# Kernel optimization log

Hardware: AMD Instinct MI355X
Metric: run time of the kernel (lower is better)

The kernel has to match this reference:

```python
import jax, jax.numpy as jnp
import numpy as np

N, E, C, NTT, NMOL = 200000, 1600000, 128, 20000, 2000
EPS = 1e-5


def setup_inputs() -> dict:
    key = jax.random.key(0)
    ks = jax.random.split(key, 32)
    s = 0.05
    d = {}
    d["node_attr"] = jax.random.normal(ks[0], (N, C), jnp.float32)
    d["adj_index"] = jax.random.randint(ks[1], (2, E), 0, N)
    d["adj_value"] = jax.random.uniform(ks[2], (E,), jnp.float32)
    d["tt_node_batch"] = jnp.sort(jax.random.randint(ks[3], (N,), 0, NTT))
    d["tt_graph_batch"] = jnp.sort(jax.random.randint(ks[4], (NTT,), 0, NMOL))
    # GCN layers (2): linear weight/bias
    d["W_gcn"] = jax.random.normal(ks[5], (2, C, C)) * s
    d["b_gcn"] = jnp.zeros((2, C))
    # 8 BatchNorm1d(C): [gcn0, gcn1, tt0, tt1, tt2, mol0, mol1, mol2] (eval mode)
    d["bn_gamma"] = jnp.ones((8, C))
    d["bn_beta"] = jnp.zeros((8, C))
    d["bn_mean"] = jnp.zeros((8, C))
    d["bn_var"] = jnp.ones((8, C))
    # 2 GATConv (tt, mol): bipartite lin_src/lin_dst, att_src/att_dst, bias (heads=1)
    d["gat_Wsrc"] = jax.random.normal(ks[6], (2, C, C)) * s
    d["gat_Wdst"] = jax.random.normal(ks[7], (2, C, C)) * s
    d["gat_asrc"] = jax.random.normal(ks[8], (2, C)) * s
    d["gat_adst"] = jax.random.normal(ks[9], (2, C)) * s
    d["gat_bias"] = jnp.zeros((2, C))
    # 2 GRUCell(C, C)
    d["gru_Wih"] = jax.random.normal(ks[10], (2, 3 * C, C)) * s
    d["gru_Whh"] = jax.random.normal(ks[11], (2, 3 * C, C)) * s
    d["gru_bih"] = jnp.zeros((2, 3 * C))
    d["gru_bhh"] = jnp.zeros((2, 3 * C))
    # predictor: 128 -> 64 (relu) -> 1
    d["pW1"] = jax.random.normal(ks[12], (64, C)) * s
    d["pb1"] = jnp.full((64,), 0.01)
    d["pW2"] = jax.random.normal(ks[13], (1, 64)) * s
    d["pb2"] = jnp.full((1,), 0.01)
    return d


def _bn(x, i, g, b, m, v):
    return (x - m[i]) * (g[i] / jnp.sqrt(v[i] + EPS)) + b[i]


def _spmm(idx, val, x, n):  # out[i] = sum_j A[i,j] x[j]
    return jax.ops.segment_sum(val[:, None] * x[idx[1]], idx[0], num_segments=n)


def _gat(x_src, x_dst, src, dst, nseg, Ws, Wd, a_s, a_d, bias):
    hs = x_src @ Ws.T
    hd = x_dst @ Wd.T
    alpha = jax.nn.leaky_relu(hs @ a_s, 0.01 * 0 + 0.01) if False else None
    a = (hs @ a_s)[src] + (hd @ a_d)[dst]
    a = jnp.where(a > 0, a, 0.01 * a)  # leaky_relu, negative_slope=0.01
    mx = jax.ops.segment_max(a, dst, num_segments=nseg)
    e = jnp.exp(a - mx[dst])
    den = jax.ops.segment_sum(e, dst, num_segments=nseg)
    w = e / den[dst]
    return jax.ops.segment_sum(w[:, None] * hs[src], dst, num_segments=nseg) + bias


def _gru(x, h, Wih, Whh, bih, bhh):
    gi = x @ Wih.T + bih
    gh = h @ Whh.T + bhh
    ir, iz, inn = jnp.split(gi, 3, axis=-1)
    hr, hz, hn = jnp.split(gh, 3, axis=-1)
    r = jax.nn.sigmoid(ir + hr)
    z = jax.nn.sigmoid(iz + hz)
    n = jnp.tanh(inn + r * hn)
    return (1.0 - z) * n + z * h


def _pool_stage(x, seg, nseg, bn_base, gi, bn_gamma, bn_beta, bn_mean, bn_var,
                gat_Wsrc, gat_Wdst, gat_asrc, gat_adst, gat_bias,
                gru_Wih, gru_Whh, gru_bih, gru_bhh):
    x = _bn(x, bn_base, bn_gamma, bn_beta, bn_mean, bn_var)
    mean = jax.ops.segment_sum(x, seg, num_segments=nseg)  # global_add_pool
    mean = _bn(jax.nn.relu(mean), bn_base + 1, bn_gamma, bn_beta, bn_mean, bn_var)
    src = jnp.arange(x.shape[0])
    g = _gat(x, mean, src, seg, nseg, gat_Wsrc[gi], gat_Wdst[gi], gat_asrc[gi], gat_adst[gi], gat_bias[gi])
    g = jax.nn.elu(g)  # dropout p=0.001 is identity in eval
    g = _gru(g, mean, gru_Wih[gi], gru_Whh[gi], gru_bih[gi], gru_bhh[gi])
    return _bn(jax.nn.relu(g), bn_base + 2, bn_gamma, bn_beta, bn_mean, bn_var)


def reference(node_attr, adj_value, W_gcn, b_gcn, bn_gamma, bn_beta, bn_mean, bn_var,
              gat_Wsrc, gat_Wdst, gat_asrc, gat_adst, gat_bias,
              gru_Wih, gru_Whh, gru_bih, gru_bhh, pW1, pb1, pW2, pb2,
              adj_index, tt_node_batch, tt_graph_batch):
    # graph embedder: two GCN layers  x <- relu(BN(A @ (x W^T) + b))
    x = node_attr
    for i in range(2):
        x = _spmm(adj_index, adj_value, x @ W_gcn[i].T, N) + b_gcn[i]
        x = jax.nn.relu(_bn(x, i, bn_gamma, bn_beta, bn_mean, bn_var))
    # tt pooling: nodes -> tt subgraphs
    tt = _pool_stage(x, tt_node_batch, NTT, 2, 0, bn_gamma, bn_beta, bn_mean, bn_var,
                     gat_Wsrc, gat_Wdst, gat_asrc, gat_adst, gat_bias,
                     gru_Wih, gru_Whh, gru_bih, gru_bhh)
    # mol pooling: tt subgraphs -> molecules
    mol = _pool_stage(tt, tt_graph_batch, NMOL, 5, 1, bn_gamma, bn_beta, bn_mean, bn_var,
                      gat_Wsrc, gat_Wdst, gat_asrc, gat_adst, gat_bias,
                      gru_Wih, gru_Whh, gru_bih, gru_bhh)
    # predictor
    h = jax.nn.relu(mol @ pW1.T + pb1)
    return h @ pW2.T + pb2  # [NMOL, 1]
```

## Files before the change

kernel.cpp:

```cpp
#include <hip/hip_runtime.h>
#include <math.h>

#define CCH 128
#define G3  384
#define BN_EPS 1e-5f
#define BSH 9
#define BROWS 512

typedef __bf16 bf16;
typedef __bf16 bf16x2 __attribute__((ext_vector_type(2)));
typedef __bf16 bf16x4 __attribute__((ext_vector_type(4)));
typedef __bf16 bf16x8 __attribute__((ext_vector_type(8)));
typedef float f32x4 __attribute__((ext_vector_type(4)));


__global__ void bnprep_kernel(const float* __restrict__ g, const float* __restrict__ b,
                              const float* __restrict__ m, const float* __restrict__ v,
                              float* __restrict__ sc, float* __restrict__ sh)
{
    int idx = blockIdx.x * 128 + threadIdx.x;
    float s = g[idx] / sqrtf(v[idx] + BN_EPS);
    sc[idx] = s;
    sh[idx] = b[idx] - m[idx] * s;
}

__global__ void f2b_kernel(const float* __restrict__ in, bf16* __restrict__ out, int n4)
{
    int i = blockIdx.x * 256 + threadIdx.x;
    if (i >= n4) return;
    float4 v = ((const float4*)in)[i];
    bf16x4 o = { (bf16)v.x, (bf16)v.y, (bf16)v.z, (bf16)v.w };
    ((bf16x4*)out)[i] = o;
}

__global__ __launch_bounds__(128) void matvec_prep_kernel(
    const float* __restrict__ Wsrc, const float* __restrict__ Wdst,
    const float* __restrict__ asrc, const float* __restrict__ adst,
    const float* __restrict__ bnsc, const float* __restrict__ bnsh,
    float* __restrict__ vsp, float* __restrict__ vd, float* __restrict__ c0)
{
    __shared__ float red[2];
    int s = blockIdx.x >> 1, which = blockIdx.x & 1;
    int k = threadIdx.x;
    const float* W = (which ? Wdst : Wsrc) + s * CCH * CCH;
    const float* a = (which ? adst : asrc) + s * CCH;
    float acc = 0.f;
    for (int j = 0; j < CCH; ++j) acc += W[j * CCH + k] * a[j];
    if (which) {
        vd[s * CCH + k] = acc;
    } else {
        int l = 2 + 3 * s;
        vsp[s * CCH + k] = acc * bnsc[l * CCH + k];
        float p = bnsh[l * CCH + k] * acc;
        for (int o = 32; o; o >>= 1) p += __shfl_down(p, o);
        if ((k & 63) == 0) red[k >> 6] = p;
        __syncthreads();
        if (k == 0) c0[s] = red[0] + red[1];
    }
}

__global__ void bounds_kernel(const int* __restrict__ batch, int n, int nseg, int* __restrict__ starts)
{
    int s = blockIdx.x * 256 + threadIdx.x;
    if (s > nseg) return;
    int lo = 0, hi = n;
    while (lo < hi) {
        int mid = (lo + hi) >> 1;
        if (batch[mid] < s) lo = mid + 1; else hi = mid;
    }
    starts[s] = lo;
}


__global__ __launch_bounds__(256) void bucket_hist_kernel(const int* __restrict__ rows,
                                                          int* __restrict__ bhist, int E)
{
    __shared__ int h[512];
    int t = threadIdx.x;
    h[t] = 0; h[t + 256] = 0;
    __syncthreads();
    int base = blockIdx.x * 4096;
#pragma unroll
    for (int i = 0; i < 16; ++i) {
        int e = base + i * 256 + t;
        if (e < E) atomicAdd(&h[rows[e] >> BSH], 1);
    }
    __syncthreads();
    if (h[t]) atomicAdd(&bhist[t], h[t]);
    if (h[t + 256]) atomicAdd(&bhist[t + 256], h[t + 256]);
}

__global__ __launch_bounds__(256) void bucket_scan_kernel(const int* __restrict__ bhist,
                                                          int* __restrict__ boff, int* __restrict__ bcur,
                                                          int* __restrict__ row_ptr, int NB, int N, int E)
{
    __shared__ int h[512], sx[512], wt[4];
    int t = threadIdx.x;
    h[t] = bhist[t]; h[t + 256] = bhist[t + 256];
    __syncthreads();
    int v0 = h[2 * t], v1 = h[2 * t + 1];
    int s = v0 + v1, incl = s;
    for (int o = 1; o < 64; o <<= 1) { int u = __shfl_up(incl, o); if ((t & 63) >= o) incl += u; }
    if ((t & 63) == 63) wt[t >> 6] = incl;
    __syncthreads();
    int woff = 0, w = t >> 6;
    for (int i = 0; i < w; ++i) woff += wt[i];
    int excl = woff + incl - s;
    sx[2 * t] = excl; sx[2 * t + 1] = excl + v0;
    __syncthreads();
    if (t < NB)       { boff[t] = sx[t];       bcur[t] = sx[t]; }
    if (t + 256 < NB) { boff[t + 256] = sx[t + 256]; bcur[t + 256] = sx[t + 256]; }
    if (t == 0) { boff[NB] = E; row_ptr[N] = E; }
}

__global__ __launch_bounds__(256) void bucket_bin_kernel(
    const int* __restrict__ rows, const int* __restrict__ cols, const float* __restrict__ val,
    int* __restrict__ bcur, int* __restrict__ brow, int2* __restrict__ bcv, int E)
{
    __shared__ int hist[512], sx[512], cnt[512], gbase[512], wt[4];
    __shared__ int mrow[4096];
    __shared__ int2 mcv[4096];
    int t = threadIdx.x;
    hist[t] = 0; hist[t + 256] = 0; cnt[t] = 0; cnt[t + 256] = 0;
    __syncthreads();
    int base = blockIdx.x * 4096;
    int r[16];
#pragma unroll
    for (int i = 0; i < 16; ++i) {
        int e = base + i * 256 + t;
        r[i] = (e < E) ? rows[e] : -1;
        if (r[i] >= 0) atomicAdd(&hist[r[i] >> BSH], 1);
    }
    __syncthreads();
    int v0 = hist[2 * t], v1 = hist[2 * t + 1];
    int s = v0 + v1, incl = s;
    for (int o = 1; o < 64; o <<= 1) { int u = __shfl_up(incl, o); if ((t & 63) >= o) incl += u; }
    if ((t & 63) == 63) wt[t >> 6] = incl;
    __syncthreads();
    int woff = 0, w = t >> 6;
    for (int i = 0; i < w; ++i) woff += wt[i];
    int excl = woff + incl - s;
    sx[2 * t] = excl; sx[2 * t + 1] = excl + v0;
    __syncthreads();
    for (int b = t; b < 512; b += 256)
        if (hist[b]) gbase[b] = atomicAdd(&bcur[b], hist[b]);
    __syncthreads();
#pragma unroll
    for (int i = 0; i < 16; ++i) {
        if (r[i] < 0) continue;
        int e = base + i * 256 + t;
        int b = r[i] >> BSH;
        int p = atomicAdd(&cnt[b], 1);
        int loc = sx[b] + p;
        mrow[loc] = r[i];
        int2 cv; cv.x = cols[e]; cv.y = __float_as_int(val[e]);
        mcv[loc] = cv;
    }
    __syncthreads();
    int Mv = sx[511] + hist[511];
    for (int loc = t; loc < Mv; loc += 256) {
        int b = mrow[loc] >> BSH;
        int g = gbase[b] + (loc - sx[b]);
        brow[g] = mrow[loc];
        bcv[g]  = mcv[loc];
    }
}

__global__ __launch_bounds__(256) void bucket_place_kernel(
    const int* __restrict__ brow, const int2* __restrict__ bcv,
    const int* __restrict__ boff, int* __restrict__ row_ptr,
    int2* __restrict__ cpack, int N)
{
    __shared__ int rcnt[512], sx[512], wt[4];
    int b = blockIdx.x;
    int t = threadIdx.x;
    rcnt[t] = 0; rcnt[t + 256] = 0;
    __syncthreads();
    int rbase = b << BSH;
    int rn = min(BROWS, N - rbase);
    int lo = boff[b], hi = boff[b + 1];
    for (int p = lo + t; p < hi; p += 256)
        atomicAdd(&rcnt[brow[p] - rbase], 1);
    __syncthreads();
    int v0 = rcnt[2 * t], v1 = rcnt[2 * t + 1];
    int s = v0 + v1, incl = s;
    for (int o = 1; o < 64; o <<= 1) { int u = __shfl_up(incl, o); if ((t & 63) >= o) incl += u; }
    if ((t & 63) == 63) wt[t >> 6] = incl;
    __syncthreads();
    int woff = 0, w = t >> 6;
    for (int i = 0; i < w; ++i) woff += wt[i];
    int excl = woff + incl - s;
    sx[2 * t] = excl; sx[2 * t + 1] = excl + v0;
    __syncthreads();
    if (t < rn)       row_ptr[rbase + t] = lo + sx[t];
    if (t + 256 < rn) row_ptr[rbase + t + 256] = lo + sx[t + 256];
    __syncthreads();
    sx[t] += lo; sx[t + 256] += lo;
    __syncthreads();
    for (int p = lo + t; p < hi; p += 256) {
        int r = brow[p];
        int slot = atomicAdd(&sx[r - rbase], 1);
        cpack[slot] = bcv[p];
    }
}


template<int IN_BF16, int OUT_BF16, int ACT>
__global__ __launch_bounds__(256, 2) void gemm_mfma(
    const void* __restrict__ Xv, const bf16* __restrict__ W,
    const float* __restrict__ bias, void* __restrict__ Yv, int M, int Nout)
{
    __shared__ bf16 Xs[128 * 136];
    __shared__ bf16 Ws[128 * 136];
    const int tid = threadIdx.x;
    const int rb = blockIdx.x * 128;
    const int cb = blockIdx.y * 128;

#pragma unroll
    for (int i = 0; i < 8; ++i) {
        int c = tid + i * 256;
        int r = c >> 4, k8 = (c & 15) << 3;
        *(bf16x8*)&Ws[r * 136 + k8] = *(const bf16x8*)&W[(size_t)(cb + r) * CCH + k8];
    }
    if (IN_BF16) {
#pragma unroll
        for (int i = 0; i < 8; ++i) {
            int c = tid + i * 256;
            int r = c >> 4, k8 = (c & 15) << 3;
            int grow = rb + r;
            bf16x8 o = {};
            if (grow < M) o = *(const bf16x8*)&((const bf16*)Xv)[(size_t)grow * CCH + k8];
            *(bf16x8*)&Xs[r * 136 + k8] = o;
        }
    } else {
#pragma unroll
        for (int i = 0; i < 16; ++i) {
            int c = tid + i * 256;
            int r = c >> 5, k4 = (c & 31) << 2;
            int grow = rb + r;
            bf16x4 o = {};
            if (grow < M) {
                float4 xv = *(const float4*)&((const float*)Xv)[(size_t)grow * CCH + k4];
                o[0] = (bf16)xv.x; o[1] = (bf16)xv.y; o[2] = (bf16)xv.z; o[3] = (bf16)xv.w;
            }
            *(bf16x4*)&Xs[r * 136 + k4] = o;
        }
    }
    __syncthreads();

    const int w = tid >> 6, lane = tid & 63;
    const int col16 = lane & 15, quad = lane >> 4;
    const int wm = (w & 1) * 64, wn = (w >> 1) * 64;

    f32x4 acc[4][4] = {};
#pragma unroll
    for (int kk = 0; kk < 4; ++kk) {
        bf16x8 af[4], bfr[4];
#pragma unroll
        for (int mi = 0; mi < 4; ++mi)
            af[mi] = *(const bf16x8*)&Xs[(wm + mi * 16 + col16) * 136 + kk * 32 + quad * 8];
#pragma unroll
        for (int ni = 0; ni < 4; ++ni)
            bfr[ni] = *(const bf16x8*)&Ws[(wn + ni * 16 + col16) * 136 + kk * 32 + quad * 8];
#pragma unroll
        for (int mi = 0; mi < 4; ++mi)
#pragma unroll
            for (int ni = 0; ni < 4; ++ni)
                acc[mi][ni] = __builtin_amdgcn_mfma_f32_16x16x32_bf16(af[mi], bfr[ni], acc[mi][ni], 0, 0, 0);
    }

#pragma unroll
    for (int mi = 0; mi < 4; ++mi) {
#pragma unroll
        for (int r = 0; r < 4; ++r) {
            int row = rb + wm + mi * 16 + quad * 4 + r;
            if (row >= M) continue;
#pragma unroll
            for (int ni = 0; ni < 4; ++ni) {
                int col = cb + wn + ni * 16 + col16;
                float v = acc[mi][ni][r];
                if (bias) v += bias[col];
                if (ACT == 1) v = v > 0.f ? v : expm1f(v);
                if (OUT_BF16) ((bf16*)Yv)[(size_t)row * Nout + col] = (bf16)v;
                else          ((float*)Yv)[(size_t)row * Nout + col] = v;
            }
        }
    }
}

template<int SCORES>
__global__ __launch_bounds__(256) void spmm_csr_kernel(
    const int* __restrict__ row_ptr, const int2* __restrict__ cpack,
    const bf16* __restrict__ Xin, bf16* __restrict__ Y,
    const float* __restrict__ bvec, const float* __restrict__ sc, const float* __restrict__ sh,
    const float* __restrict__ vsp, const float* __restrict__ c0p, float* __restrict__ scores,
    int Nrow)
{
    int gid = blockIdx.x * 256 + threadIdx.x;
    int row = gid >> 4;
    if (row >= Nrow) return;
    int l8 = (gid & 15) << 3;
    int st = row_ptr[row], en = row_ptr[row + 1];
    float acc[8] = {};
    int j = st;
    for (; j + 2 <= en; j += 2) {
        int2 p0 = cpack[j];
        int2 p1 = cpack[j + 1];
        bf16x8 x0 = *(const bf16x8*)&Xin[(size_t)p0.x * CCH + l8];
        bf16x8 x1 = *(const bf16x8*)&Xin[(size_t)p1.x * CCH + l8];
        float v0 = __int_as_float(p0.y), v1 = __int_as_float(p1.y);
#pragma unroll
        for (int q = 0; q < 8; ++q) acc[q] += v0 * (float)x0[q] + v1 * (float)x1[q];
    }
    if (j < en) {
        int2 p0 = cpack[j];
        bf16x8 x0 = *(const bf16x8*)&Xin[(size_t)p0.x * CCH + l8];
        float v0 = __int_as_float(p0.y);
#pragma unroll
        for (int q = 0; q < 8; ++q) acc[q] += v0 * (float)x0[q];
    }
    float o[8];
    bf16x8 ov;
#pragma unroll
    for (int q = 0; q < 8; ++q) {
        o[q] = fmaxf((acc[q] + bvec[l8 + q]) * sc[l8 + q] + sh[l8 + q], 0.f);
        ov[q] = (bf16)o[q];
    }
    *(bf16x8*)&Y[(size_t)row * CCH + l8] = ov;
    if (SCORES) {
        float p = 0.f;
#pragma unroll
        for (int q = 0; q < 8; ++q) p += o[q] * vsp[l8 + q];
        for (int d = 8; d; d >>= 1) p += __shfl_down(p, d, 16);
        if ((gid & 15) == 0) scores[row] = p + c0p[0];
    }
}

__global__ __launch_bounds__(128) void segstage_kernel(
    const bf16* __restrict__ X, const float* __restrict__ sarr, const int* __restrict__ starts,
    const float* __restrict__ sc2, const float* __restrict__ sh2,
    const float* __restrict__ sc3, const float* __restrict__ sh3,
    const float* __restrict__ vd, float* __restrict__ mean, float* __restrict__ upool)
{
    __shared__ float red[2];
    __shared__ float adsh;
    int t = blockIdx.x;
    int c = threadIdx.x;
    int st = starts[t], en = starts[t + 1];
    float sum = 0.f;
    for (int i = st; i < en; ++i) sum += (float)X[(size_t)i * CCH + c];
    float cnt = (float)(en - st);
    float poolb = fmaxf(sum * sc2[c] + cnt * sh2[c], 0.f);
    float mv = poolb * sc3[c] + sh3[c];
    mean[(size_t)t * CCH + c] = mv;
    float p = mv * vd[c];
    for (int o = 32; o; o >>= 1) p += __shfl_down(p, o);
    if ((c & 63) == 0) red[c >> 6] = p;
    __syncthreads();
    if (c == 0) adsh = red[0] + red[1];
    __syncthreads();
    if (en == st) { upool[(size_t)t * CCH + c] = 0.f; return; }
    float adt = adsh;
    float lm = -3.0e38f;
    for (int i = st + c; i < en; i += 128) {
        float a = sarr[i] + adt;
        a = a > 0.f ? a : 0.01f * a;
        lm = fmaxf(lm, a);
    }
    for (int o = 32; o; o >>= 1) lm = fmaxf(lm, __shfl_down(lm, o));
    if ((c & 63) == 0) red[c >> 6] = lm;
    __syncthreads();
    float m = fmaxf(red[0], red[1]);
    float u = 0.f, den = 0.f;
    for (int i = st; i < en; ++i) {
        float a = sarr[i] + adt;
        a = a > 0.f ? a : 0.01f * a;
        float e = __expf(a - m);
        den += e;
        u += e * (float)X[(size_t)i * CCH + c];
    }
    upool[(size_t)t * CCH + c] = (u / den) * sc2[c] + sh2[c];
}

template<int OUT_BF16, int SCORES>
__global__ __launch_bounds__(256) void gru_kernel(
    const float* __restrict__ giM, const float* __restrict__ ghM, const float* __restrict__ mean,
    const float* __restrict__ sc4, const float* __restrict__ sh4,
    void* __restrict__ out,
    const float* __restrict__ vsp2, const float* __restrict__ c02, float* __restrict__ scores,
    int total)
{
    __shared__ float sred[4];
    int idx = blockIdx.x * 256 + threadIdx.x;
    bool ok = idx < total;
    int t = idx >> 7, c = idx & 127;
    float o = 0.f;
    if (ok) {
        size_t b = (size_t)t * G3;
        float ir = giM[b + c],  iz = giM[b + 128 + c], inn = giM[b + 256 + c];
        float hr = ghM[b + c],  hz = ghM[b + 128 + c], hn  = ghM[b + 256 + c];
        float r = 1.f / (1.f + __expf(-(ir + hr)));
        float z = 1.f / (1.f + __expf(-(iz + hz)));
        float nn = tanhf(inn + r * hn);
        float h = (1.f - z) * nn + z * mean[idx];
        h = fmaxf(h, 0.f);
        o = h * sc4[c] + sh4[c];
        if (OUT_BF16) ((bf16*)out)[idx] = (bf16)o;
        else          ((float*)out)[idx] = o;
    }
    if (SCORES) {
        float p = ok ? o * vsp2[c] : 0.f;
        for (int d = 32; d; d >>= 1) p += __shfl_down(p, d);
        int w = threadIdx.x >> 6;
        if ((threadIdx.x & 63) == 0) sred[w] = p;
        __syncthreads();
        if (threadIdx.x == 0 && ok)   scores[t] = sred[0] + sred[1] + c02[0];
        if (threadIdx.x == 128 && ok) scores[t] = sred[2] + sred[3] + c02[0];
    }
}

__global__ __launch_bounds__(64) void pred_kernel(
    const float* __restrict__ mol, const float* __restrict__ pW1, const float* __restrict__ pb1,
    const float* __restrict__ pW2, const float* __restrict__ pb2, float* __restrict__ out)
{
    __shared__ float row[CCH];
    int m = blockIdx.x;
    int j = threadIdx.x;
    row[j] = mol[(size_t)m * CCH + j];
    row[j + 64] = mol[(size_t)m * CCH + 64 + j];
    __syncthreads();
    float h = pb1[j];
#pragma unroll
    for (int k = 0; k < CCH; ++k) h += row[k] * pW1[j * CCH + k];
    h = fmaxf(h, 0.f);
    float p = h * pW2[j];
    for (int o = 32; o; o >>= 1) p += __shfl_down(p, o);
    if (j == 0) out[m] = p + pb2[0];
}


extern "C" void kernel_launch(void* const* d_in, const int* in_sizes, int n_in,
                              void* d_out, int out_size, void* d_ws, size_t ws_size,
                              hipStream_t stream)
{
    (void)n_in; (void)ws_size;
    const float* node_attr      = (const float*)d_in[0];
    const int*   adj_index      = (const int*)  d_in[1];
    const float* adj_value      = (const float*)d_in[2];
    const int*   tt_node_batch  = (const int*)  d_in[3];
    const int*   tt_graph_batch = (const int*)  d_in[4];
    const float* W_gcn    = (const float*)d_in[5];
    const float* b_gcn    = (const float*)d_in[6];
    const float* bn_gamma = (const float*)d_in[7];
    const float* bn_beta  = (const float*)d_in[8];
    const float* bn_mean  = (const float*)d_in[9];
    const float* bn_var   = (const float*)d_in[10];
    const float* gat_Wsrc = (const float*)d_in[11];
    const float* gat_Wdst = (const float*)d_in[12];
    const float* gat_asrc = (const float*)d_in[13];
    const float* gat_adst = (const float*)d_in[14];
    const float* gat_bias = (const float*)d_in[15];
    const float* gru_Wih  = (const float*)d_in[16];
    const float* gru_Whh  = (const float*)d_in[17];
    const float* gru_bih  = (const float*)d_in[18];
    const float* gru_bhh  = (const float*)d_in[19];
    const float* pW1 = (const float*)d_in[20];
    const float* pb1 = (const float*)d_in[21];
    const float* pW2 = (const float*)d_in[22];
    const float* pb2 = (const float*)d_in[23];

    const int E    = in_sizes[2];
    const int N    = in_sizes[3];
    const int NTT  = in_sizes[4];
    const int NMOL = out_size;
    const int NB   = (N + BROWS - 1) >> BSH;

    const int* adj_rows = adj_index;
    const int* adj_cols = adj_index + E;

    char* wsb = (char*)d_ws;
    size_t off = 0;
    auto carve = [&](size_t bytes) -> char* {
        char* p = wsb + off;
        off = (off + bytes + 255) & ~(size_t)255;
        return p;
    };
    bf16* bufB = (bf16*)carve((size_t)N * CCH * 2);
    bf16* bufA = (bf16*)carve((size_t)N * CCH * 2);
    bf16* tt   = (bf16*)carve((size_t)NTT * CCH * 2);
    float* mol  = (float*)carve((size_t)NMOL * CCH * 4);
    float* mean  = (float*)carve((size_t)NTT * CCH * 4);
    float* upool = (float*)carve((size_t)NTT * CCH * 4);
    float* gbuf  = (float*)carve((size_t)NTT * CCH * 4);
    float* giM   = (float*)carve((size_t)NTT * G3 * 4);
    float* ghM   = (float*)carve((size_t)NTT * G3 * 4);
    float* scores = (float*)carve((size_t)N * 4);
    int* starts_tt  = (int*)carve((size_t)(NTT + 1) * 4);
    int* starts_mol = (int*)carve((size_t)(NMOL + 1) * 4);
    float* bnsc = (float*)carve(8 * CCH * 4);
    float* bnsh = (float*)carve(8 * CCH * 4);
    float* vsp  = (float*)carve(2 * CCH * 4);
    float* vd   = (float*)carve(2 * CCH * 4);
    float* c0   = (float*)carve(2 * 4);
    bf16* Wgcnb = (bf16*)carve((size_t)2 * CCH * CCH * 2);
    bf16* Wsrcb = (bf16*)carve((size_t)2 * CCH * CCH * 2);
    bf16* Wihb  = (bf16*)carve((size_t)2 * G3 * CCH * 2);
    bf16* Whhb  = (bf16*)carve((size_t)2 * G3 * CCH * 2);
    int*   bhist   = (int*)carve(512 * 4);
    int*   boff    = (int*)carve((size_t)(NB + 1) * 4);
    int*   bcur    = (int*)carve((size_t)NB * 4);
    int*   row_ptr = (int*)carve((size_t)(N + 1) * 4);
    int*   brow    = (int*)carve((size_t)E * 4);
    int2*  bcv     = (int2*)carve((size_t)E * 8);
    int2*  cpack   = (int2*)carve((size_t)E * 8);

    bnprep_kernel<<<8, 128, 0, stream>>>(bn_gamma, bn_beta, bn_mean, bn_var, bnsc, bnsh);
    matvec_prep_kernel<<<4, 128, 0, stream>>>(gat_Wsrc, gat_Wdst, gat_asrc, gat_adst,
                                              bnsc, bnsh, vsp, vd, c0);
    {
        int n4;
        n4 = 2 * CCH * CCH / 4; f2b_kernel<<<(n4 + 255) / 256, 256, 0, stream>>>(W_gcn, Wgcnb, n4);
        n4 = 2 * CCH * CCH / 4; f2b_kernel<<<(n4 + 255) / 256, 256, 0, stream>>>(gat_Wsrc, Wsrcb, n4);
        n4 = 2 * G3 * CCH / 4;  f2b_kernel<<<(n4 + 255) / 256, 256, 0, stream>>>(gru_Wih, Wihb, n4);
        n4 = 2 * G3 * CCH / 4;  f2b_kernel<<<(n4 + 255) / 256, 256, 0, stream>>>(gru_Whh, Whhb, n4);
    }
    bounds_kernel<<<(NTT + 1 + 255) / 256, 256, 0, stream>>>(tt_node_batch, N, NTT, starts_tt);
    bounds_kernel<<<(NMOL + 1 + 255) / 256, 256, 0, stream>>>(tt_graph_batch, NTT, NMOL, starts_mol);

    const int nchunk = (E + 4095) / 4096;
    hipMemsetAsync(bhist, 0, 512 * 4, stream);
    bucket_hist_kernel<<<nchunk, 256, 0, stream>>>(adj_rows, bhist, E);
    bucket_scan_kernel<<<1, 256, 0, stream>>>(bhist, boff, bcur, row_ptr, NB, N, E);
    bucket_bin_kernel<<<nchunk, 256, 0, stream>>>(adj_rows, adj_cols, adj_value,
                                                  bcur, brow, bcv, E);
    bucket_place_kernel<<<NB, 256, 0, stream>>>(brow, bcv, boff, row_ptr, cpack, N);

    dim3 gg((N + 127) / 128, 1);
    const int spmm_blocks = ((size_t)N * 16 + 255) / 256;
    gemm_mfma<0, 1, 0><<<gg, 256, 0, stream>>>(node_attr, Wgcnb, nullptr, bufB, N, CCH);
    spmm_csr_kernel<0><<<spmm_blocks, 256, 0, stream>>>(
        row_ptr, cpack, bufB, bufA, b_gcn, bnsc, bnsh, nullptr, nullptr, nullptr, N);
    gemm_mfma<1, 1, 0><<<gg, 256, 0, stream>>>(bufA, Wgcnb + CCH * CCH, nullptr, bufB, N, CCH);
    spmm_csr_kernel<1><<<spmm_blocks, 256, 0, stream>>>(
        row_ptr, cpack, bufB, bufA, b_gcn + CCH, bnsc + CCH, bnsh + CCH,
        vsp, c0, scores, N);

    {
        int bnb = 2, gi = 0, nseg = NTT;
        segstage_kernel<<<nseg, 128, 0, stream>>>(bufA, scores, starts_tt,
            bnsc + bnb * CCH, bnsh + bnb * CCH, bnsc + (bnb + 1) * CCH, bnsh + (bnb + 1) * CCH,
            vd + gi * CCH, mean, upool);
        dim3 g1((nseg + 127) / 128, 1);
        gemm_mfma<0, 0, 1><<<g1, 256, 0, stream>>>(upool, Wsrcb + gi * CCH * CCH,
                                                   gat_bias + gi * CCH, gbuf, nseg, CCH);
        dim3 g2((nseg + 127) / 128, 3);
        gemm_mfma<0, 0, 0><<<g2, 256, 0, stream>>>(gbuf, Wihb + gi * G3 * CCH,
                                                   gru_bih + gi * G3, giM, nseg, G3);
        gemm_mfma<0, 0, 0><<<g2, 256, 0, stream>>>(mean, Whhb + gi * G3 * CCH,
                                                   gru_bhh + gi * G3, ghM, nseg, G3);
        gru_kernel<1, 1><<<(nseg * CCH + 255) / 256, 256, 0, stream>>>(giM, ghM, mean,
            bnsc + (bnb + 2) * CCH, bnsh + (bnb + 2) * CCH, tt,
            vsp + CCH, c0 + 1, scores, nseg * CCH);
    }

    {
        int bnb = 5, gi = 1, nseg = NMOL;
        segstage_kernel<<<nseg, 128, 0, stream>>>(tt, scores, starts_mol,
            bnsc + bnb * CCH, bnsh + bnb * CCH, bnsc + (bnb + 1) * CCH, bnsh + (bnb + 1) * CCH,
            vd + gi * CCH, mean, upool);
        dim3 g1((nseg + 127) / 128, 1);
        gemm_mfma<0, 0, 1><<<g1, 256, 0, stream>>>(upool, Wsrcb + gi * CCH * CCH,
                                                   gat_bias + gi * CCH, gbuf, nseg, CCH);
        dim3 g2((nseg + 127) / 128, 3);
        gemm_mfma<0, 0, 0><<<g2, 256, 0, stream>>>(gbuf, Wihb + gi * G3 * CCH,
                                                   gru_bih + gi * G3, giM, nseg, G3);
        gemm_mfma<0, 0, 0><<<g2, 256, 0, stream>>>(mean, Whhb + gi * G3 * CCH,
                                                   gru_bhh + gi * G3, ghM, nseg, G3);
        gru_kernel<0, 0><<<(nseg * CCH + 255) / 256, 256, 0, stream>>>(giM, ghM, mean,
            bnsc + (bnb + 2) * CCH, bnsh + (bnb + 2) * CCH, mol,
            nullptr, nullptr, nullptr, nseg * CCH);
    }

    pred_kernel<<<NMOL, 64, 0, stream>>>(mol, pW1, pb1, pW2, pb2, (float*)d_out);
}
```

Baseline: 688.6 us.

## Fuse prep kernels, pack row into column bits, merge GRU GEMMs and predictor

Merges the BN prep, matvec prep, bounds search, histogram memset and weight bf16 conversions into one multi-role launch. Drops the separate row array in CSR construction by packing the in-bucket row index into the high bits of the column word. Fuses the two GRU GEMMs into a single dual launch and fuses the final GRU with the predictor MLP. It also unrolls the SpMM inner loop to four edges. The aim is fewer launches and less memory traffic in the preprocessing, at the cost of relying on column indices fitting in 19 bits.

```diff
diff --git a/kernel.cpp b/kernel.cpp
--- a/kernel.cpp
+++ b/kernel.cpp
@@ -6,6 +6,7 @@
 #define BN_EPS 1e-5f
 #define BSH 9
 #define BROWS 512
+#define COLBITS 19
 
 typedef __bf16 bf16;
 typedef __bf16 bf16x2 __attribute__((ext_vector_type(2)));
@@ -13,62 +14,81 @@
 typedef __bf16 bf16x8 __attribute__((ext_vector_type(8)));
 typedef float f32x4 __attribute__((ext_vector_type(4)));
 
-
-__global__ void bnprep_kernel(const float* __restrict__ g, const float* __restrict__ b,
-                              const float* __restrict__ m, const float* __restrict__ v,
-                              float* __restrict__ sc, float* __restrict__ sh)
-{
-    int idx = blockIdx.x * 128 + threadIdx.x;
-    float s = g[idx] / sqrtf(v[idx] + BN_EPS);
-    sc[idx] = s;
-    sh[idx] = b[idx] - m[idx] * s;
-}
-
-__global__ void f2b_kernel(const float* __restrict__ in, bf16* __restrict__ out, int n4)
-{
-    int i = blockIdx.x * 256 + threadIdx.x;
-    if (i >= n4) return;
-    float4 v = ((const float4*)in)[i];
-    bf16x4 o = { (bf16)v.x, (bf16)v.y, (bf16)v.z, (bf16)v.w };
-    ((bf16x4*)out)[i] = o;
-}
-
-__global__ __launch_bounds__(128) void matvec_prep_kernel(
+__global__ __launch_bounds__(256) void prep_kernel(
+    const float* __restrict__ g, const float* __restrict__ b,
+    const float* __restrict__ m, const float* __restrict__ v,
+    float* __restrict__ bnsc, float* __restrict__ bnsh,
     const float* __restrict__ Wsrc, const float* __restrict__ Wdst,
     const float* __restrict__ asrc, const float* __restrict__ adst,
-    const float* __restrict__ bnsc, const float* __restrict__ bnsh,
-    float* __restrict__ vsp, float* __restrict__ vd, float* __restrict__ c0)
+    float* __restrict__ vsp, float* __restrict__ vd, float* __restrict__ c0,
+    const int* __restrict__ tt_node_batch, int N, int NTT, int* __restrict__ starts_tt,
+    const int* __restrict__ tt_graph_batch, int NMOL, int* __restrict__ starts_mol,
+    int* __restrict__ bhist,
+    const float* __restrict__ Wgcn, bf16* __restrict__ Wgcnb,
+    bf16* __restrict__ Wsrcb,
+    const float* __restrict__ Wih, bf16* __restrict__ Wihb,
+    const float* __restrict__ Whh, bf16* __restrict__ Whhb,
+    int B1, int B2, int B3, int B4, int B5, int B6, int B7, int B8)
 {
     __shared__ float red[2];
-    int s = blockIdx.x >> 1, which = blockIdx.x & 1;
-    int k = threadIdx.x;
-    const float* W = (which ? Wdst : Wsrc) + s * CCH * CCH;
-    const float* a = (which ? adst : asrc) + s * CCH;
-    float acc = 0.f;
-    for (int j = 0; j < CCH; ++j) acc += W[j * CCH + k] * a[j];
-    if (which) {
-        vd[s * CCH + k] = acc;
+    const int bid = blockIdx.x;
+    const int tid = threadIdx.x;
+    if (bid < B1) {
+        int idx = bid * 256 + tid;
+        if (idx < 8 * CCH) {
+            float s = g[idx] / sqrtf(v[idx] + BN_EPS);
+            bnsc[idx] = s;
+            bnsh[idx] = b[idx] - m[idx] * s;
+        }
+    } else if (bid < B2) {
+        int s = bid - B1;
+        int which = tid >> 7, k = tid & 127;
+        const float* W = (which ? Wdst : Wsrc) + s * CCH * CCH;
+        const float* a = (which ? adst : asrc) + s * CCH;
+        float acc = 0.f;
+        for (int j = 0; j < CCH; ++j) acc += W[j * CCH + k] * a[j];
+        if (which) {
+            vd[s * CCH + k] = acc;
+        } else {
+            int l = 2 + 3 * s;
+            float scl = g[l * CCH + k] / sqrtf(v[l * CCH + k] + BN_EPS);
+            float shf = b[l * CCH + k] - m[l * CCH + k] * scl;
+            vsp[s * CCH + k] = acc * scl;
+            float p = shf * acc;
+            for (int o = 32; o; o >>= 1) p += __shfl_down(p, o);
+            if ((k & 63) == 0) red[k >> 6] = p;
+        }
+        __syncthreads();
+        if (tid == 0) c0[s] = red[0] + red[1];
+    } else if (bid < B3) {
+        int s = (bid - B2) * 256 + tid;
+        if (s <= NTT) {
+            int lo = 0, hi = N;
+            while (lo < hi) { int mid = (lo + hi) >> 1; if (tt_node_batch[mid] < s) lo = mid + 1; else hi = mid; }
+            starts_tt[s] = lo;
+        }
+    } else if (bid < B4) {
+        int s = (bid - B3) * 256 + tid;
+        if (s <= NMOL) {
+            int lo = 0, hi = NTT;
+            while (lo < hi) { int mid = (lo + hi) >> 1; if (tt_graph_batch[mid] < s) lo = mid + 1; else hi = mid; }
+            starts_mol[s] = lo;
+        }
+    } else if (bid < B5) {
+        bhist[tid] = 0; bhist[tid + 256] = 0;
     } else {
-        int l = 2 + 3 * s;
-        vsp[s * CCH + k] = acc * bnsc[l * CCH + k];
-        float p = bnsh[l * CCH + k] * acc;
-        for (int o = 32; o; o >>= 1) p += __shfl_down(p, o);
-        if ((k & 63) == 0) red[k >> 6] = p;
-        __syncthreads();
-        if (k == 0) c0[s] = red[0] + red[1];
-    }
-}
-
-__global__ void bounds_kernel(const int* __restrict__ batch, int n, int nseg, int* __restrict__ starts)
-{
-    int s = blockIdx.x * 256 + threadIdx.x;
-    if (s > nseg) return;
-    int lo = 0, hi = n;
-    while (lo < hi) {
-        int mid = (lo + hi) >> 1;
-        if (batch[mid] < s) lo = mid + 1; else hi = mid;
-    }
-    starts[s] = lo;
+        const float* src; bf16* dst; int i0, n4;
+        if (bid < B6)      { src = Wgcn; dst = Wgcnb; i0 = (bid - B5) * 256; n4 = 2 * CCH * CCH / 4; }
+        else if (bid < B7) { src = Wsrc; dst = Wsrcb; i0 = (bid - B6) * 256; n4 = 2 * CCH * CCH / 4; }
+        else if (bid < B8) { src = Wih;  dst = Wihb;  i0 = (bid - B7) * 256; n4 = 2 * G3 * CCH / 4; }
+        else               { src = Whh;  dst = Whhb;  i0 = (bid - B8) * 256; n4 = 2 * G3 * CCH / 4; }
+        int i = i0 + tid;
+        if (i < n4) {
+            float4 x = ((const float4*)src)[i];
+            bf16x4 o = { (bf16)x.x, (bf16)x.y, (bf16)x.z, (bf16)x.w };
+            ((bf16x4*)dst)[i] = o;
+        }
+    }
 }
 
 
@@ -115,10 +135,10 @@
 
 __global__ __launch_bounds__(256) void bucket_bin_kernel(
     const int* __restrict__ rows, const int* __restrict__ cols, const float* __restrict__ val,
-    int* __restrict__ bcur, int* __restrict__ brow, int2* __restrict__ bcv, int E)
+    int* __restrict__ bcur, int2* __restrict__ bcv, int E)
 {
     __shared__ int hist[512], sx[512], cnt[512], gbase[512], wt[4];
-    __shared__ int mrow[4096];
+    __shared__ int mb[4096];
     __shared__ int2 mcv[4096];
     int t = threadIdx.x;
     hist[t] = 0; hist[t + 256] = 0; cnt[t] = 0; cnt[t + 256] = 0;
@@ -142,33 +162,33 @@
     int excl = woff + incl - s;
     sx[2 * t] = excl; sx[2 * t + 1] = excl + v0;
     __syncthreads();
-    for (int b = t; b < 512; b += 256)
-        if (hist[b]) gbase[b] = atomicAdd(&bcur[b], hist[b]);
+    for (int bb = t; bb < 512; bb += 256)
+        if (hist[bb]) gbase[bb] = atomicAdd(&bcur[bb], hist[bb]);
     __syncthreads();
 #pragma unroll
     for (int i = 0; i < 16; ++i) {
         if (r[i] < 0) continue;
         int e = base + i * 256 + t;
-        int b = r[i] >> BSH;
-        int p = atomicAdd(&cnt[b], 1);
-        int loc = sx[b] + p;
-        mrow[loc] = r[i];
-        int2 cv; cv.x = cols[e]; cv.y = __float_as_int(val[e]);
+        int bb = r[i] >> BSH;
+        int p = atomicAdd(&cnt[bb], 1);
+        int loc = sx[bb] + p;
+        mb[loc] = bb;
+        int2 cv;
+        cv.x = cols[e] | ((r[i] & (BROWS - 1)) << COLBITS);
+        cv.y = __float_as_int(val[e]);
         mcv[loc] = cv;
     }
     __syncthreads();
     int Mv = sx[511] + hist[511];
     for (int loc = t; loc < Mv; loc += 256) {
-        int b = mrow[loc] >> BSH;
-        int g = gbase[b] + (loc - sx[b]);
-        brow[g] = mrow[loc];
-        bcv[g]  = mcv[loc];
+        int bb = mb[loc];
+        int gidx = gbase[bb] + (loc - sx[bb]);
+        bcv[gidx] = mcv[loc];
     }
 }
 
 __global__ __launch_bounds__(256) void bucket_place_kernel(
-    const int* __restrict__ brow, const int2* __restrict__ bcv,
-    const int* __restrict__ boff, int* __restrict__ row_ptr,
+    const int2* __restrict__ bcv, const int* __restrict__ boff, int* __restrict__ row_ptr,
     int2* __restrict__ cpack, int N)
 {
     __shared__ int rcnt[512], sx[512], wt[4];
@@ -180,7 +200,7 @@
     int rn = min(BROWS, N - rbase);
     int lo = boff[b], hi = boff[b + 1];
     for (int p = lo + t; p < hi; p += 256)
-        atomicAdd(&rcnt[brow[p] - rbase], 1);
+        atomicAdd(&rcnt[((unsigned)bcv[p].x) >> COLBITS], 1);
     __syncthreads();
     int v0 = rcnt[2 * t], v1 = rcnt[2 * t + 1];
     int s = v0 + v1, incl = s;
@@ -198,12 +218,13 @@
     sx[t] += lo; sx[t + 256] += lo;
     __syncthreads();
     for (int p = lo + t; p < hi; p += 256) {
-        int r = brow[p];
-        int slot = atomicAdd(&sx[r - rbase], 1);
-        cpack[slot] = bcv[p];
-    }
-}
-
+        int2 cv = bcv[p];
+        int rin = ((unsigned)cv.x) >> COLBITS;
+        int slot = atomicAdd(&sx[rin], 1);
+        cv.x &= (1 << COLBITS) - 1;
+        cpack[slot] = cv;
+    }
+}
 
 template<int IN_BF16, int OUT_BF16, int ACT>
 __global__ __launch_bounds__(256, 2) void gemm_mfma(
@@ -278,11 +299,82 @@
 #pragma unroll
             for (int ni = 0; ni < 4; ++ni) {
                 int col = cb + wn + ni * 16 + col16;
-                float v = acc[mi][ni][r];
-                if (bias) v += bias[col];
-                if (ACT == 1) v = v > 0.f ? v : expm1f(v);
-                if (OUT_BF16) ((bf16*)Yv)[(size_t)row * Nout + col] = (bf16)v;
-                else          ((float*)Yv)[(size_t)row * Nout + col] = v;
+                float vv = acc[mi][ni][r];
+                if (bias) vv += bias[col];
+                if (ACT == 1) vv = vv > 0.f ? vv : expm1f(vv);
+                if (OUT_BF16) ((bf16*)Yv)[(size_t)row * Nout + col] = (bf16)vv;
+                else          ((float*)Yv)[(size_t)row * Nout + col] = vv;
+            }
+        }
+    }
+}
+
+__global__ __launch_bounds__(256, 2) void gemm_dual(
+    const float* __restrict__ X0, const bf16* __restrict__ W0,
+    const float* __restrict__ b0, float* __restrict__ Y0,
+    const float* __restrict__ X1, const bf16* __restrict__ W1,
+    const float* __restrict__ b1, float* __restrict__ Y1, int M)
+{
+    __shared__ bf16 Xs[128 * 136];
+    __shared__ bf16 Ws[128 * 136];
+    const int tid = threadIdx.x;
+    const int rb = blockIdx.x * 128;
+    const int yy = blockIdx.y;
+    const float* X; const bf16* W; const float* bias; float* Y; int cb;
+    if (yy < 3) { X = X0; W = W0; bias = b0; Y = Y0; cb = yy * 128; }
+    else        { X = X1; W = W1; bias = b1; Y = Y1; cb = (yy - 3) * 128; }
+
+#pragma unroll
+    for (int i = 0; i < 8; ++i) {
+        int c = tid + i * 256;
+        int r = c >> 4, k8 = (c & 15) << 3;
+        *(bf16x8*)&Ws[r * 136 + k8] = *(const bf16x8*)&W[(size_t)(cb + r) * CCH + k8];
+    }
+#pragma unroll
+    for (int i = 0; i < 16; ++i) {
+        int c = tid + i * 256;
+        int r = c >> 5, k4 = (c & 31) << 2;
+        int grow = rb + r;
+        bf16x4 o = {};
+        if (grow < M) {
+            float4 xv = *(const float4*)&X[(size_t)grow * CCH + k4];
+            o[0] = (bf16)xv.x; o[1] = (bf16)xv.y; o[2] = (bf16)xv.z; o[3] = (bf16)xv.w;
+        }
+        *(bf16x4*)&Xs[r * 136 + k4] = o;
+    }
+    __syncthreads();
+
+    const int w = tid >> 6, lane = tid & 63;
+    const int col16 = lane & 15, quad = lane >> 4;
+    const int wm = (w & 1) * 64, wn = (w >> 1) * 64;
+
+    f32x4 acc[4][4] = {};
+#pragma unroll
+    for (int kk = 0; kk < 4; ++kk) {
+        bf16x8 af[4], bfr[4];
+#pragma unroll
+        for (int mi = 0; mi < 4; ++mi)
+            af[mi] = *(const bf16x8*)&Xs[(wm + mi * 16 + col16) * 136 + kk * 32 + quad * 8];
+#pragma unroll
+        for (int ni = 0; ni < 4; ++ni)
+            bfr[ni] = *(const bf16x8*)&Ws[(wn + ni * 16 + col16) * 136 + kk * 32 + quad * 8];
+#pragma unroll
+        for (int mi = 0; mi < 4; ++mi)
+#pragma unroll
+            for (int ni = 0; ni < 4; ++ni)
+                acc[mi][ni] = __builtin_amdgcn_mfma_f32_16x16x32_bf16(af[mi], bfr[ni], acc[mi][ni], 0, 0, 0);
+    }
+
+#pragma unroll
+    for (int mi = 0; mi < 4; ++mi) {
+#pragma unroll
+        for (int r = 0; r < 4; ++r) {
+            int row = rb + wm + mi * 16 + quad * 4 + r;
+            if (row >= M) continue;
+#pragma unroll
+            for (int ni = 0; ni < 4; ++ni) {
+                int col = cb + wn + ni * 16 + col16;
+                Y[(size_t)row * G3 + col] = acc[mi][ni][r] + bias[col];
             }
         }
     }
@@ -303,14 +395,26 @@
     int st = row_ptr[row], en = row_ptr[row + 1];
     float acc[8] = {};
     int j = st;
-    for (; j + 2 <= en; j += 2) {
-        int2 p0 = cpack[j];
-        int2 p1 = cpack[j + 1];
+    for (; j + 4 <= en; j += 4) {
+        int2 p0 = cpack[j], p1 = cpack[j + 1], p2 = cpack[j + 2], p3 = cpack[j + 3];
+        bf16x8 x0 = *(const bf16x8*)&Xin[(size_t)p0.x * CCH + l8];
+        bf16x8 x1 = *(const bf16x8*)&Xin[(size_t)p1.x * CCH + l8];
+        bf16x8 x2 = *(const bf16x8*)&Xin[(size_t)p2.x * CCH + l8];
+        bf16x8 x3 = *(const bf16x8*)&Xin[(size_t)p3.x * CCH + l8];
+        float v0 = __int_as_float(p0.y), v1 = __int_as_float(p1.y);
+        float v2 = __int_as_float(p2.y), v3 = __int_as_float(p3.y);
+#pragma unroll
+        for (int q = 0; q < 8; ++q)
+            acc[q] += v0 * (float)x0[q] + v1 * (float)x1[q] + v2 * (float)x2[q] + v3 * (float)x3[q];
+    }
+    if (j + 2 <= en) {
+        int2 p0 = cpack[j], p1 = cpack[j + 1];
         bf16x8 x0 = *(const bf16x8*)&Xin[(size_t)p0.x * CCH + l8];
         bf16x8 x1 = *(const bf16x8*)&Xin[(size_t)p1.x * CCH + l8];
         float v0 = __int_as_float(p0.y), v1 = __int_as_float(p1.y);
 #pragma unroll
         for (int q = 0; q < 8; ++q) acc[q] += v0 * (float)x0[q] + v1 * (float)x1[q];
+        j += 2;
     }
     if (j < en) {
         int2 p0 = cpack[j];
@@ -382,11 +486,10 @@
     upool[(size_t)t * CCH + c] = (u / den) * sc2[c] + sh2[c];
 }
 
-template<int OUT_BF16, int SCORES>
 __global__ __launch_bounds__(256) void gru_kernel(
     const float* __restrict__ giM, const float* __restrict__ ghM, const float* __restrict__ mean,
     const float* __restrict__ sc4, const float* __restrict__ sh4,
-    void* __restrict__ out,
+    bf16* __restrict__ out,
     const float* __restrict__ vsp2, const float* __restrict__ c02, float* __restrict__ scores,
     int total)
 {
@@ -405,37 +508,52 @@
         float h = (1.f - z) * nn + z * mean[idx];
         h = fmaxf(h, 0.f);
         o = h * sc4[c] + sh4[c];
-        if (OUT_BF16) ((bf16*)out)[idx] = (bf16)o;
-        else          ((float*)out)[idx] = o;
-    }
-    if (SCORES) {
-        float p = ok ? o * vsp2[c] : 0.f;
+        out[idx] = (bf16)o;
+    }
+    float p = ok ? o * vsp2[c] : 0.f;
+    for (int d = 32; d; d >>= 1) p += __shfl_down(p, d);
+    int w = threadIdx.x >> 6;
+    if ((threadIdx.x & 63) == 0) sred[w] = p;
+    __syncthreads();
+    if (threadIdx.x == 0 && ok)   scores[t] = sred[0] + sred[1] + c02[0];
+    if (threadIdx.x == 128 && ok) scores[t] = sred[2] + sred[3] + c02[0];
+}
+
+__global__ __launch_bounds__(256) void gru_pred_kernel(
+    const float* __restrict__ giM, const float* __restrict__ ghM, const float* __restrict__ mean,
+    const float* __restrict__ sc4, const float* __restrict__ sh4,
+    const float* __restrict__ pW1, const float* __restrict__ pb1,
+    const float* __restrict__ pW2, const float* __restrict__ pb2,
+    float* __restrict__ out, int nseg)
+{
+    __shared__ float row[2][CCH];
+    int half = threadIdx.x >> 7;
+    int c = threadIdx.x & 127;
+    int t = blockIdx.x * 2 + half;
+    bool ok = t < nseg;
+    float o = 0.f;
+    if (ok) {
+        size_t b = (size_t)t * G3;
+        float ir = giM[b + c],  iz = giM[b + 128 + c], inn = giM[b + 256 + c];
+        float hr = ghM[b + c],  hz = ghM[b + 128 + c], hn  = ghM[b + 256 + c];
+        float r = 1.f / (1.f + __expf(-(ir + hr)));
+        float z = 1.f / (1.f + __expf(-(iz + hz)));
+        float nn = tanhf(inn + r * hn);
+        float h = (1.f - z) * nn + z * mean[(size_t)t * CCH + c];
+        h = fmaxf(h, 0.f);
+        o = h * sc4[c] + sh4[c];
+    }
+    row[half][c] = o;
+    __syncthreads();
+    if (c < 64 && ok) {
+        float h = pb1[c];
+#pragma unroll
+        for (int k = 0; k < CCH; ++k) h += row[half][k] * pW1[c * CCH + k];
+        h = fmaxf(h, 0.f);
+        float p = h * pW2[c];
         for (int d = 32; d; d >>= 1) p += __shfl_down(p, d);
-        int w = threadIdx.x >> 6;
-        if ((threadIdx.x & 63) == 0) sred[w] = p;
-        __syncthreads();
-        if (threadIdx.x == 0 && ok)   scores[t] = sred[0] + sred[1] + c02[0];
-        if (threadIdx.x == 128 && ok) scores[t] = sred[2] + sred[3] + c02[0];
-    }
-}
-
-__global__ __launch_bounds__(64) void pred_kernel(
-    const float* __restrict__ mol, const float* __restrict__ pW1, const float* __restrict__ pb1,
-    const float* __restrict__ pW2, const float* __restrict__ pb2, float* __restrict__ out)
-{
-    __shared__ float row[CCH];
-    int m = blockIdx.x;
-    int j = threadIdx.x;
-    row[j] = mol[(size_t)m * CCH + j];
-    row[j + 64] = mol[(size_t)m * CCH + 64 + j];
-    __syncthreads();
-    float h = pb1[j];
-#pragma unroll
-    for (int k = 0; k < CCH; ++k) h += row[k] * pW1[j * CCH + k];
-    h = fmaxf(h, 0.f);
-    float p = h * pW2[j];
-    for (int o = 32; o; o >>= 1) p += __shfl_down(p, o);
-    if (j == 0) out[m] = p + pb2[0];
+        if (c == 0) out[t] = p + pb2[0];
+    }
 }
 
 
@@ -488,7 +606,6 @@
     bf16* bufB = (bf16*)carve((size_t)N * CCH * 2);
     bf16* bufA = (bf16*)carve((size_t)N * CCH * 2);
     bf16* tt   = (bf16*)carve((size_t)NTT * CCH * 2);
-    float* mol  = (float*)carve((size_t)NMOL * CCH * 4);
     float* mean  = (float*)carve((size_t)NTT * CCH * 4);
     float* upool = (float*)carve((size_t)NTT * CCH * 4);
     float* gbuf  = (float*)carve((size_t)NTT * CCH * 4);
@@ -510,30 +627,32 @@
     int*   boff    = (int*)carve((size_t)(NB + 1) * 4);
     int*   bcur    = (int*)carve((size_t)NB * 4);
     int*   row_ptr = (int*)carve((size_t)(N + 1) * 4);
-    int*   brow    = (int*)carve((size_t)E * 4);
     int2*  bcv     = (int2*)carve((size_t)E * 8);
     int2*  cpack   = (int2*)carve((size_t)E * 8);
 
-    bnprep_kernel<<<8, 128, 0, stream>>>(bn_gamma, bn_beta, bn_mean, bn_var, bnsc, bnsh);
-    matvec_prep_kernel<<<4, 128, 0, stream>>>(gat_Wsrc, gat_Wdst, gat_asrc, gat_adst,
-                                              bnsc, bnsh, vsp, vd, c0);
-    {
-        int n4;
-        n4 = 2 * CCH * CCH / 4; f2b_kernel<<<(n4 + 255) / 256, 256, 0, stream>>>(W_gcn, Wgcnb, n4);
-        n4 = 2 * CCH * CCH / 4; f2b_kernel<<<(n4 + 255) / 256, 256, 0, stream>>>(gat_Wsrc, Wsrcb, n4);
-        n4 = 2 * G3 * CCH / 4;  f2b_kernel<<<(n4 + 255) / 256, 256, 0, stream>>>(gru_Wih, Wihb, n4);
-        n4 = 2 * G3 * CCH / 4;  f2b_kernel<<<(n4 + 255) / 256, 256, 0, stream>>>(gru_Whh, Whhb, n4);
-    }
-    bounds_kernel<<<(NTT + 1 + 255) / 256, 256, 0, stream>>>(tt_node_batch, N, NTT, starts_tt);
-    bounds_kernel<<<(NMOL + 1 + 255) / 256, 256, 0, stream>>>(tt_graph_batch, NTT, NMOL, starts_mol);
+    const int B1 = 4;
+    const int B2 = B1 + 2;
+    const int B3 = B2 + (NTT + 1 + 255) / 256;
+    const int B4 = B3 + (NMOL + 1 + 255) / 256;
+    const int B5 = B4 + 1;
+    const int B6 = B5 + 32;
+    const int B7 = B6 + 32;
+    const int B8 = B7 + 96;
+    const int B9 = B8 + 96;
+    prep_kernel<<<B9, 256, 0, stream>>>(
+        bn_gamma, bn_beta, bn_mean, bn_var, bnsc, bnsh,
+        gat_Wsrc, gat_Wdst, gat_asrc, gat_adst, vsp, vd, c0,
+        tt_node_batch, N, NTT, starts_tt,
+        tt_graph_batch, NMOL, starts_mol,
+        bhist,
+        W_gcn, Wgcnb, Wsrcb, gru_Wih, Wihb, gru_Whh, Whhb,
+        B1, B2, B3, B4, B5, B6, B7, B8);
 
     const int nchunk = (E + 4095) / 4096;
-    hipMemsetAsync(bhist, 0, 512 * 4, stream);
     bucket_hist_kernel<<<nchunk, 256, 0, stream>>>(adj_rows, bhist, E);
     bucket_scan_kernel<<<1, 256, 0, stream>>>(bhist, boff, bcur, row_ptr, NB, N, E);
-    bucket_bin_kernel<<<nchunk, 256, 0, stream>>>(adj_rows, adj_cols, adj_value,
-                                                  bcur, brow, bcv, E);
-    bucket_place_kernel<<<NB, 256, 0, stream>>>(brow, bcv, boff, row_ptr, cpack, N);
+    bucket_bin_kernel<<<nchunk, 256, 0, stream>>>(adj_rows, adj_cols, adj_value, bcur, bcv, E);
+    bucket_place_kernel<<<NB, 256, 0, stream>>>(bcv, boff, row_ptr, cpack, N);
 
     dim3 gg((N + 127) / 128, 1);
     const int spmm_blocks = ((size_t)N * 16 + 255) / 256;
@@ -546,40 +665,34 @@
         vsp, c0, scores, N);
 
     {
-        int bnb = 2, gi = 0, nseg = NTT;
+        const int bnb = 2, gi = 0, nseg = NTT;
         segstage_kernel<<<nseg, 128, 0, stream>>>(bufA, scores, starts_tt,
             bnsc + bnb * CCH, bnsh + bnb * CCH, bnsc + (bnb + 1) * CCH, bnsh + (bnb + 1) * CCH,
             vd + gi * CCH, mean, upool);
         dim3 g1((nseg + 127) / 128, 1);
         gemm_mfma<0, 0, 1><<<g1, 256, 0, stream>>>(upool, Wsrcb + gi * CCH * CCH,
                                                    gat_bias + gi * CCH, gbuf, nseg, CCH);
-        dim3 g2((nseg + 127) / 128, 3);
-        gemm_mfma<0, 0, 0><<<g2, 256, 0, stream>>>(gbuf, Wihb + gi * G3 * CCH,
-                                                   gru_bih + gi * G3, giM, nseg, G3);
-        gemm_mfma<0, 0, 0><<<g2, 256, 0, stream>>>(mean, Whhb + gi * G3 * CCH,
-                                                   gru_bhh + gi * G3, ghM, nseg, G3);
-        gru_kernel<1, 1><<<(nseg * CCH + 255) / 256, 256, 0, stream>>>(giM, ghM, mean,
+        dim3 g2((nseg + 127) / 128, 6);
+        gemm_dual<<<g2, 256, 0, stream>>>(gbuf, Wihb + gi * G3 * CCH, gru_bih + gi * G3, giM,
+                                          mean, Whhb + gi * G3 * CCH, gru_bhh + gi * G3, ghM, nseg);
+        gru_kernel<<<(nseg * CCH + 255) / 256, 256, 0, stream>>>(giM, ghM, mean,
             bnsc + (bnb + 2) * CCH, bnsh + (bnb + 2) * CCH, tt,
             vsp + CCH, c0 + 1, scores, nseg * CCH);
     }
 
     {
-        int bnb = 5, gi = 1, nseg = NMOL;
+        const int bnb = 5, gi = 1, nseg = NMOL;
         segstage_kernel<<<nseg, 128, 0, stream>>>(tt, scores, starts_mol,
             bnsc + bnb * CCH, bnsh + bnb * CCH, bnsc + (bnb + 1) * CCH, bnsh + (bnb + 1) * CCH,
             vd + gi * CCH, mean, upool);
         dim3 g1((nseg + 127) / 128, 1);
         gemm_mfma<0, 0, 1><<<g1, 256, 0, stream>>>(upool, Wsrcb + gi * CCH * CCH,
                                                    gat_bias + gi * CCH, gbuf, nseg, CCH);
-        dim3 g2((nseg + 127) / 128, 3);
-        gemm_mfma<0, 0, 0><<<g2, 256, 0, stream>>>(gbuf, Wihb + gi * G3 * CCH,
-                                                   gru_bih + gi * G3, giM, nseg, G3);
-        gemm_mfma<0, 0, 0><<<g2, 256, 0, stream>>>(mean, Whhb + gi * G3 * CCH,
-                                                   gru_bhh + gi * G3, ghM, nseg, G3);
-        gru_kernel<0, 0><<<(nseg * CCH + 255) / 256, 256, 0, stream>>>(giM, ghM, mean,
-            bnsc + (bnb + 2) * CCH, bnsh + (bnb + 2) * CCH, mol,
-            nullptr, nullptr, nullptr, nseg * CCH);
-    }
-
-    pred_kernel<<<NMOL, 64, 0, stream>>>(mol, pW1, pb1, pW2, pb2, (float*)d_out);
-}
+        dim3 g2((nseg + 127) / 128, 6);
+        gemm_dual<<<g2, 256, 0, stream>>>(gbuf, Wihb + gi * G3 * CCH, gru_bih + gi * G3, giM,
+                                          mean, Whhb + gi * G3 * CCH, gru_bhh + gi * G3, ghM, nseg);
+        gru_pred_kernel<<<(nseg + 1) / 2, 256, 0, stream>>>(giM, ghM, mean,
+            bnsc + (bnb + 2) * CCH, bnsh + (bnb + 2) * CCH,
+            pW1, pb1, pW2, pb2, (float*)d_out, nseg);
+    }
+}
```

Measured after the change: 612.4 us. 1.12x faster.
